# Kernel tuning notes

Measured on AMD Instinct MI355X. Metric: run time of the kernel, lower is better.

Reference implementation:

```python
import jax, jax.numpy as jnp
import numpy as np

EPS = 1e-9
ROUTING_ITERS = 3


def _squash_elem(s):
    # Faithful to source: squash over trailing axis of size 1 => elementwise.
    sq = s * s
    return (sq / (1.0 + sq)) * s / jnp.sqrt(sq + EPS)


def setup_inputs() -> dict:
    key = jax.random.key(0)
    k1, k2 = jax.random.split(key)
    B, I, P = 16, 2048, 16   # batch, num_input_capsules, input_dim_capsules
    O, D = 64, 32            # num_capsules, dim_capsules
    x = jax.random.normal(k1, (B, I, P), dtype=jnp.float32)
    # glorot-ish scale for the transformation weights
    W = jax.random.normal(k2, (1, I, O, D, P), dtype=jnp.float32) * (1.0 / np.sqrt(P))
    bias = jnp.zeros((1, 1, O, D, 1), dtype=jnp.float32)
    return {"x": x, "W": W, "bias": bias}


def reference(x, W, bias):
    # u_hat[b,i,o,d] = sum_p W[0,i,o,d,p] * x[b,i,p]  (the tile+mul+reduce in TF)
    u_hat = jnp.einsum('bip,iodp->biod', x, W[0])
    B, I, O, _ = u_hat.shape
    bias_od = bias[0, 0, :, :, 0]               # [O, D]
    b_logits = jnp.zeros((B, I, O), dtype=u_hat.dtype)
    v = None
    for it in range(ROUTING_ITERS):
        c = jax.nn.softmax(b_logits, axis=2)     # softmax over output capsules
        s = jnp.einsum('bio,biod->bod', c, u_hat) + bias_od
        v = _squash_elem(s)                      # [B, O, D]
        if it < ROUTING_ITERS - 1:
            # agreement[b,i,o] = sum_d u_hat[b,i,o,d] * v[b,o,d]
            b_logits = b_logits + jnp.einsum('biod,bod->bio', u_hat, v)
    return v  # [B, num_capsules, dim_capsules]
```

## Files before the change

kernel.cpp:

```cpp
#include <hip/hip_runtime.h>

#define B_ 16
#define I_ 2048
#define OD_ 2048
#define EPSQ 1e-9f

__device__ __forceinline__ float squashf(float s) {
  float sq = s * s;
  return sq / (1.0f + sq) * s * rsqrtf(sq + EPSQ);
}

__global__ __launch_bounds__(256) void k_uhat(
    const float* __restrict__ x, const float* __restrict__ W,
    float* __restrict__ u, float* __restrict__ part0)
{
  const int t = threadIdx.x;
  const int q = blockIdx.x & 3;
  const int ic = blockIdx.x >> 2;
  const int i0 = ic * 8;
  const int pr = q * 256 + t;

  float s0a[B_], s0b[B_];
#pragma unroll
  for (int b = 0; b < B_; ++b) { s0a[b] = 0.f; s0b[b] = 0.f; }

  for (int ii = 0; ii < 8; ++ii) {
    const int i = i0 + ii;
    const float4* wp = (const float4*)(W + (size_t)(i * OD_ + pr * 2) * 16);
    float4 w[8];
#pragma unroll
    for (int k = 0; k < 8; ++k) w[k] = wp[k];

#pragma unroll
    for (int b = 0; b < B_; ++b) {
      const float4* xp = (const float4*)(x + (size_t)(b * I_ + i) * 16);
      float u0 = 0.f, u1 = 0.f;
#pragma unroll
      for (int qq = 0; qq < 4; ++qq) {
        float4 xq = xp[qq];
        float4 wa = w[qq], wb = w[qq + 4];
        u0 += xq.x * wa.x + xq.y * wa.y + xq.z * wa.z + xq.w * wa.w;
        u1 += xq.x * wb.x + xq.y * wb.y + xq.z * wb.z + xq.w * wb.w;
      }
      float2 uv; uv.x = u0; uv.y = u1;
      *(float2*)(u + (size_t)(b * I_ + i) * OD_ + pr * 2) = uv;
      s0a[b] += u0; s0b[b] += u1;
    }
  }
#pragma unroll
  for (int b = 0; b < B_; ++b) {
    float2 sv; sv.x = s0a[b]; sv.y = s0b[b];
    ((float2*)part0)[(size_t)(ic * B_ + b) * 1024 + pr] = sv;
  }
}

__global__ __launch_bounds__(256) void k_s0red(
    const float* __restrict__ part0, float* __restrict__ s0)
{
  const int b = blockIdx.x >> 3;
  const int od = (blockIdx.x & 7) * 256 + threadIdx.x;
  float a = 0.f;
  const float* p = part0 + (size_t)b * OD_ + od;
  for (int ic = 0; ic < 256; ++ic) a += p[(size_t)ic * B_ * OD_];
  s0[b * OD_ + od] = a;
}

__global__ __launch_bounds__(256, 3) void k_route(
    const float* __restrict__ u,
    const float* __restrict__ sA, float scaleA,
    const float* __restrict__ sB,
    const float* __restrict__ bias,
    float* __restrict__ part)
{
  __shared__ float red[4 * 2048];
  const int t = threadIdx.x;
  const int o = t & 63;
  const int wv = t >> 6;
  const int b = blockIdx.x >> 6;
  const int i0 = ((blockIdx.x & 63) * 4 + wv) * 8;

  float vv[32];
  {
    const int base = b * OD_ + o * 32;
#pragma unroll
    for (int d = 0; d < 32; ++d) {
      float bs = bias[o * 32 + d];
      float val = squashf(sA[base + d] * scaleA + bs);
      if (sB) val += squashf(sB[base + d] + bs);
      vv[d] = val;
    }
  }
  float acc[32];
#pragma unroll
  for (int d = 0; d < 32; ++d) acc[d] = 0.f;

  for (int ii = 0; ii < 8; ++ii) {
    const int i = i0 + ii;
    const float4* up = (const float4*)(u + (size_t)(b * I_ + i) * OD_ + o * 32);
    float uf[32];
#pragma unroll
    for (int qq = 0; qq < 8; ++qq) {
      float4 r = up[qq];
      uf[4 * qq + 0] = r.x; uf[4 * qq + 1] = r.y;
      uf[4 * qq + 2] = r.z; uf[4 * qq + 3] = r.w;
    }
    float logit = 0.f;
#pragma unroll
    for (int d = 0; d < 32; ++d) logit = fmaf(uf[d], vv[d], logit);
    float m = logit;
#pragma unroll
    for (int off = 32; off > 0; off >>= 1) m = fmaxf(m, __shfl_xor(m, off, 64));
    float e = __expf(logit - m);
    float sm = e;
#pragma unroll
    for (int off = 32; off > 0; off >>= 1) sm += __shfl_xor(sm, off, 64);
    float c = e / sm;
#pragma unroll
    for (int d = 0; d < 32; ++d) acc[d] = fmaf(c, uf[d], acc[d]);
  }

#pragma unroll
  for (int d = 0; d < 32; ++d) red[wv * 2048 + d * 64 + o] = acc[d];
  __syncthreads();
#pragma unroll
  for (int k = 0; k < 8; ++k) {
    int od = t * 8 + k;
    int oo = od >> 5, dd = od & 31;
    int a = dd * 64 + oo;
    part[(size_t)blockIdx.x * OD_ + od] =
        red[a] + red[2048 + a] + red[4096 + a] + red[6144 + a];
  }
}

__global__ __launch_bounds__(256) void k_s1red(
    const float* __restrict__ part, float* __restrict__ s1)
{
  const int b = blockIdx.x >> 3;
  const int od = (blockIdx.x & 7) * 256 + threadIdx.x;
  float a = 0.f;
  const float* p = part + (size_t)b * 64 * OD_ + od;
#pragma unroll 4
  for (int g = 0; g < 64; ++g) a += p[(size_t)g * OD_];
  s1[b * OD_ + od] = a;
}

__global__ __launch_bounds__(256) void k_outred(
    const float* __restrict__ part, const float* __restrict__ bias,
    float* __restrict__ out)
{
  const int b = blockIdx.x >> 3;
  const int od = (blockIdx.x & 7) * 256 + threadIdx.x;
  float a = 0.f;
  const float* p = part + (size_t)b * 64 * OD_ + od;
#pragma unroll 4
  for (int g = 0; g < 64; ++g) a += p[(size_t)g * OD_];
  out[b * OD_ + od] = squashf(a + bias[od]);
}

extern "C" void kernel_launch(void* const* d_in, const int* in_sizes, int n_in,
                              void* d_out, int out_size, void* d_ws, size_t ws_size,
                              hipStream_t stream) {
  const float* x = (const float*)d_in[0];
  const float* W = (const float*)d_in[1];
  const float* bias = (const float*)d_in[2];
  float* out = (float*)d_out;

  char* ws = (char*)d_ws;
  float* u_ws  = (float*)ws;
  float* part0 = (float*)(ws + 268435456ull);
  float* part1 = (float*)(ws + 302055424ull);
  float* part2 = (float*)(ws + 310444032ull);
  float* s0    = (float*)(ws + 318832640ull);
  float* s1    = s0 + 32768;

  k_uhat <<<dim3(1024), dim3(256), 0, stream>>>(x, W, u_ws, part0);
  k_s0red<<<dim3(128),  dim3(256), 0, stream>>>(part0, s0);
  k_route<<<dim3(1024), dim3(256), 0, stream>>>(u_ws, s0, 1.0f / 64.0f, nullptr, bias, part1);
  k_s1red<<<dim3(128),  dim3(256), 0, stream>>>(part1, s1);
  k_route<<<dim3(1024), dim3(256), 0, stream>>>(u_ws, s0, 1.0f / 64.0f, s1, bias, part2);
  k_outred<<<dim3(128), dim3(256), 0, stream>>>(part2, bias, out);
}
```

Before: 623.0 us.

## Restructure routing kernel to single-wave blocks without shared-memory reduction

The routing kernel now uses one 64-thread wave per block, with each block covering 16 input capsules and writing its partial sums straight to global memory. This removes the LDS transpose and the __syncthreads. In exchange there are twice as many partials (128 per batch), so the reduction kernels now sum 128 slices, and part2 reuses the part0 buffer. Smaller tweaks: nontemporal loads of W in the u_hat kernel, a fast reciprocal in the softmax, occupancy hints, and reduction loop unroll pragmas.

```diff
diff --git a/kernel.cpp b/kernel.cpp
--- a/kernel.cpp
+++ b/kernel.cpp
@@ -5,12 +5,14 @@
 #define OD_ 2048
 #define EPSQ 1e-9f
 
+typedef float v4f __attribute__((ext_vector_type(4)));
+
 __device__ __forceinline__ float squashf(float s) {
   float sq = s * s;
   return sq / (1.0f + sq) * s * rsqrtf(sq + EPSQ);
 }
 
-__global__ __launch_bounds__(256) void k_uhat(
+__global__ __launch_bounds__(256, 4) void k_uhat(
     const float* __restrict__ x, const float* __restrict__ W,
     float* __restrict__ u, float* __restrict__ part0)
 {
@@ -26,19 +28,19 @@
 
   for (int ii = 0; ii < 8; ++ii) {
     const int i = i0 + ii;
-    const float4* wp = (const float4*)(W + (size_t)(i * OD_ + pr * 2) * 16);
-    float4 w[8];
+    const v4f* wp = (const v4f*)(W + (size_t)(i * OD_ + pr * 2) * 16);
+    v4f w[8];
 #pragma unroll
-    for (int k = 0; k < 8; ++k) w[k] = wp[k];
+    for (int k = 0; k < 8; ++k) w[k] = __builtin_nontemporal_load(wp + k);
 
 #pragma unroll
     for (int b = 0; b < B_; ++b) {
-      const float4* xp = (const float4*)(x + (size_t)(b * I_ + i) * 16);
+      const v4f* xp = (const v4f*)(x + (size_t)(b * I_ + i) * 16);
       float u0 = 0.f, u1 = 0.f;
 #pragma unroll
       for (int qq = 0; qq < 4; ++qq) {
-        float4 xq = xp[qq];
-        float4 wa = w[qq], wb = w[qq + 4];
+        v4f xq = xp[qq];
+        v4f wa = w[qq], wb = w[qq + 4];
         u0 += xq.x * wa.x + xq.y * wa.y + xq.z * wa.z + xq.w * wa.w;
         u1 += xq.x * wb.x + xq.y * wb.y + xq.z * wb.z + xq.w * wb.w;
       }
@@ -61,52 +63,56 @@
   const int od = (blockIdx.x & 7) * 256 + threadIdx.x;
   float a = 0.f;
   const float* p = part0 + (size_t)b * OD_ + od;
+#pragma unroll 8
   for (int ic = 0; ic < 256; ++ic) a += p[(size_t)ic * B_ * OD_];
   s0[b * OD_ + od] = a;
 }
 
-__global__ __launch_bounds__(256, 3) void k_route(
+__global__ __launch_bounds__(64, 2) void k_route(
     const float* __restrict__ u,
     const float* __restrict__ sA, float scaleA,
     const float* __restrict__ sB,
     const float* __restrict__ bias,
     float* __restrict__ part)
 {
-  __shared__ float red[4 * 2048];
-  const int t = threadIdx.x;
-  const int o = t & 63;
-  const int wv = t >> 6;
-  const int b = blockIdx.x >> 6;
-  const int i0 = ((blockIdx.x & 63) * 4 + wv) * 8;
+  const int o = threadIdx.x;
+  const int b = blockIdx.x >> 7;
+  const int g = blockIdx.x & 127;
+  const int i0 = g * 16;
 
-  float vv[32];
+  v4f vv[8], acc[8];
   {
-    const int base = b * OD_ + o * 32;
+    const float* sa = sA + b * OD_ + o * 32;
+    const float* sb = sB ? sB + b * OD_ + o * 32 : nullptr;
+    const float* bp = bias + o * 32;
 #pragma unroll
-    for (int d = 0; d < 32; ++d) {
-      float bs = bias[o * 32 + d];
-      float val = squashf(sA[base + d] * scaleA + bs);
-      if (sB) val += squashf(sB[base + d] + bs);
-      vv[d] = val;
+    for (int qq = 0; qq < 8; ++qq) {
+#pragma unroll
+      for (int j = 0; j < 4; ++j) {
+        float bs = bp[qq * 4 + j];
+        float val = squashf(sa[qq * 4 + j] * scaleA + bs);
+        if (sb) val += squashf(sb[qq * 4 + j] + bs);
+        vv[qq][j] = val;
+      }
+      v4f z = {0.f, 0.f, 0.f, 0.f};
+      acc[qq] = z;
     }
   }
-  float acc[32];
+
+  for (int ii = 0; ii < 16; ++ii) {
+    const int i = i0 + ii;
+    const v4f* up = (const v4f*)(u + (size_t)(b * I_ + i) * OD_ + o * 32);
+    v4f r[8];
 #pragma unroll
-  for (int d = 0; d < 32; ++d) acc[d] = 0.f;
+    for (int qq = 0; qq < 8; ++qq) r[qq] = up[qq];
 
-  for (int ii = 0; ii < 8; ++ii) {
-    const int i = i0 + ii;
-    const float4* up = (const float4*)(u + (size_t)(b * I_ + i) * OD_ + o * 32);
-    float uf[32];
-#pragma unroll
-    for (int qq = 0; qq < 8; ++qq) {
-      float4 r = up[qq];
-      uf[4 * qq + 0] = r.x; uf[4 * qq + 1] = r.y;
-      uf[4 * qq + 2] = r.z; uf[4 * qq + 3] = r.w;
-    }
     float logit = 0.f;
 #pragma unroll
-    for (int d = 0; d < 32; ++d) logit = fmaf(uf[d], vv[d], logit);
+    for (int qq = 0; qq < 8; ++qq)
+#pragma unroll
+      for (int j = 0; j < 4; ++j)
+        logit = fmaf(r[qq][j], vv[qq][j], logit);
+
     float m = logit;
 #pragma unroll
     for (int off = 32; off > 0; off >>= 1) m = fmaxf(m, __shfl_xor(m, off, 64));
@@ -114,22 +120,18 @@
     float sm = e;
 #pragma unroll
     for (int off = 32; off > 0; off >>= 1) sm += __shfl_xor(sm, off, 64);
-    float c = e / sm;
+    float c = e * __builtin_amdgcn_rcpf(sm);
+
 #pragma unroll
-    for (int d = 0; d < 32; ++d) acc[d] = fmaf(c, uf[d], acc[d]);
+    for (int qq = 0; qq < 8; ++qq)
+#pragma unroll
+      for (int j = 0; j < 4; ++j)
+        acc[qq][j] = fmaf(c, r[qq][j], acc[qq][j]);
   }
 
+  v4f* pp = (v4f*)(part + (size_t)(b * 128 + g) * OD_ + o * 32);
 #pragma unroll
-  for (int d = 0; d < 32; ++d) red[wv * 2048 + d * 64 + o] = acc[d];
-  __syncthreads();
-#pragma unroll
-  for (int k = 0; k < 8; ++k) {
-    int od = t * 8 + k;
-    int oo = od >> 5, dd = od & 31;
-    int a = dd * 64 + oo;
-    part[(size_t)blockIdx.x * OD_ + od] =
-        red[a] + red[2048 + a] + red[4096 + a] + red[6144 + a];
-  }
+  for (int qq = 0; qq < 8; ++qq) pp[qq] = acc[qq];
 }
 
 __global__ __launch_bounds__(256) void k_s1red(
@@ -138,9 +140,9 @@
   const int b = blockIdx.x >> 3;
   const int od = (blockIdx.x & 7) * 256 + threadIdx.x;
   float a = 0.f;
-  const float* p = part + (size_t)b * 64 * OD_ + od;
-#pragma unroll 4
-  for (int g = 0; g < 64; ++g) a += p[(size_t)g * OD_];
+  const float* p = part + (size_t)b * 128 * OD_ + od;
+#pragma unroll 8
+  for (int g = 0; g < 128; ++g) a += p[(size_t)g * OD_];
   s1[b * OD_ + od] = a;
 }
 
@@ -151,9 +153,9 @@
   const int b = blockIdx.x >> 3;
   const int od = (blockIdx.x & 7) * 256 + threadIdx.x;
   float a = 0.f;
-  const float* p = part + (size_t)b * 64 * OD_ + od;
-#pragma unroll 4
-  for (int g = 0; g < 64; ++g) a += p[(size_t)g * OD_];
+  const float* p = part + (size_t)b * 128 * OD_ + od;
+#pragma unroll 8
+  for (int g = 0; g < 128; ++g) a += p[(size_t)g * OD_];
   out[b * OD_ + od] = squashf(a + bias[od]);
 }
 
@@ -168,15 +170,15 @@
   char* ws = (char*)d_ws;
   float* u_ws  = (float*)ws;
   float* part0 = (float*)(ws + 268435456ull);
-  float* part1 = (float*)(ws + 302055424ull);
-  float* part2 = (float*)(ws + 310444032ull);
-  float* s0    = (float*)(ws + 318832640ull);
+  float* part1 = (float*)(ws + 301989888ull);
+  float* part2 = part0;
+  float* s0    = (float*)(ws + 318767104ull);
   float* s1    = s0 + 32768;
 
   k_uhat <<<dim3(1024), dim3(256), 0, stream>>>(x, W, u_ws, part0);
   k_s0red<<<dim3(128),  dim3(256), 0, stream>>>(part0, s0);
-  k_route<<<dim3(1024), dim3(256), 0, stream>>>(u_ws, s0, 1.0f / 64.0f, nullptr, bias, part1);
+  k_route<<<dim3(2048), dim3(64),  0, stream>>>(u_ws, s0, 1.0f / 64.0f, nullptr, bias, part1);
   k_s1red<<<dim3(128),  dim3(256), 0, stream>>>(part1, s1);
-  k_route<<<dim3(1024), dim3(256), 0, stream>>>(u_ws, s0, 1.0f / 64.0f, s1, bias, part2);
+  k_route<<<dim3(2048), dim3(64),  0, stream>>>(u_ws, s0, 1.0f / 64.0f, s1, bias, part2);
   k_outred<<<dim3(128), dim3(256), 0, stream>>>(part2, bias, out);
 }
```

New measurement: 677.9 us. +8.8%, slower.
